# Kernel tuning notes

Measured on AMD Instinct MI355X. Metric: run time of the kernel, lower is better.

The kernel has to match this reference:

```python
import jax, jax.numpy as jnp
import numpy as np

N = 1536       # n_nodes
D_IN = 256     # in_features
D_OUT = 64     # out_features (= n_hidden, n_heads=1, is_concat=True)
N_WAY = 16     # known_attacks_count
SLOPE = 0.2    # LeakyReLU negative slope


def setup_inputs() -> dict:
    key = jax.random.key(0)
    k1, k2, k3, k4, k5 = jax.random.split(key, 5)
    hidden_vectors = jax.random.normal(k1, (N, D_IN), dtype=jnp.float32)
    labels = jax.random.randint(k2, (N, 1), 0, N_WAY)
    zda_mask = jax.random.randint(k3, (N, 1), 0, 2).astype(bool)
    # deterministic support/query split: first half support, last half query
    query_mask = jnp.concatenate([jnp.zeros(N // 2, bool), jnp.ones(N // 2, bool)])
    W = jax.random.normal(k4, (D_OUT, D_IN), jnp.float32) * (1.0 / np.sqrt(D_IN))
    attn_w = jax.random.normal(k5, (D_OUT,), jnp.float32) * (1.0 / np.sqrt(D_OUT))
    return {"hidden_vectors": hidden_vectors, "W": W, "attn_w": attn_w,
            "labels": labels, "zda_mask": zda_mask, "query_mask": query_mask,
            "known_attacks_count": N_WAY}


def _forward(hidden_vectors, W, attn_w, labels, zda_mask, n_way):
    n = hidden_vectors.shape[0]
    dt = hidden_vectors.dtype
    # one-hot labels (scatter equivalent)
    oh = jax.nn.one_hot(labels[:, 0], n_way, dtype=dt)                 # [n, n_way]
    known = ~zda_mask[:, 0]                                            # unknown == zda
    ohm = jnp.where(known[:, None], oh, jnp.zeros((), dt))             # masked one-hot
    # collaborative kernel: semantic similarity between known pairs, else 1
    sem = ohm @ ohm.T                                                  # [n, n]
    cond = known[:, None] & known[None, :]
    kernel = jnp.where(cond, sem, jnp.ones((), dt))
    # GATv2 with shared weights, 1 head: e[i,j] = attn . lrelu(g[i] + g[j])
    g = hidden_vectors @ W.T                                           # [n, d_out]
    s = g[:, None, :] + g[None, :, :]                                  # [n, n, d_out]
    s = jnp.where(s >= 0, s, SLOPE * s)                                # LeakyReLU
    e = jnp.einsum('ijd,d->ij', s, attn_w)                             # [n, n]
    e = jnp.where(kernel == 0.0, -jnp.inf, e)                          # colaborative mask
    a = jax.nn.softmax(e, axis=1)                                      # [n, n]
    h_out = a @ g                                                      # [n, d_out] (concat, 1 head)
    # centroids over support nodes (first half)
    n_sup = n // 2
    h_sup, oh_sup = h_out[:n_sup], oh[:n_sup]
    agg = oh_sup.T @ h_sup                                             # [n_way, d_out]
    counts = oh_sup.sum(0)                                             # [n_way]
    centroids = jnp.where((counts > 0)[:, None],
                          agg / jnp.maximum(counts, 1.0)[:, None], 0.0)
    # inverse euclidean distance scores for query nodes (last half)
    hq = h_out[n_sup:]
    d2 = (jnp.sum(hq * hq, 1)[:, None] + jnp.sum(centroids * centroids, 1)[None, :]
          - 2.0 * hq @ centroids.T)
    dist = jnp.sqrt(jnp.maximum(d2, 0.0))
    scores = 1.0 / (dist + 1e-10)
    return scores, h_out, a


def reference(hidden_vectors, W, attn_w, labels, zda_mask, query_mask, known_attacks_count):
    return _forward(hidden_vectors, W, attn_w, labels, zda_mask, known_attacks_count)
```

## Files before the change

kernel.cpp:

```cpp
#include <hip/hip_runtime.h>
#include <math.h>

#define NN 1536
#define DIN 256
#define DOUT 64
#define NWAY 16
#define NSUP 768
#define IB 12
#define JBLK 256
#define SROWS 6

#define OFF_SCORES 0
#define OFF_H 12288
#define OFF_A 110592

#define WG 0
#define WQ 98304
#define WCODE 99840
#define WCENT 101376

__global__ __launch_bounds__(256) void k_g(const float* __restrict__ hid,
                                           const float* __restrict__ W,
                                           const float* __restrict__ attw,
                                           const int* __restrict__ labels,
                                           const int* __restrict__ zda,
                                           float* __restrict__ g,
                                           float* __restrict__ q,
                                           int* __restrict__ code) {
  int t = threadIdx.x;
  int r = t >> 6, d = t & 63;
  int i = blockIdx.x * 4 + r;
  const float4* hp = (const float4*)(hid + (size_t)i * DIN);
  const float4* wp = (const float4*)(W + (size_t)d * DIN);
  float4 acc = {0.f, 0.f, 0.f, 0.f};
#pragma unroll
  for (int k = 0; k < DIN / 4; k++) {
    float4 h4 = hp[k];
    float4 w4 = wp[k];
    acc.x = fmaf(h4.x, w4.x, acc.x);
    acc.y = fmaf(h4.y, w4.y, acc.y);
    acc.z = fmaf(h4.z, w4.z, acc.z);
    acc.w = fmaf(h4.w, w4.w, acc.w);
  }
  float gv = (acc.x + acc.y) + (acc.z + acc.w);
  g[(size_t)i * DOUT + d] = gv;
  float val = gv * attw[d];
#pragma unroll
  for (int off = 32; off >= 1; off >>= 1) val += __shfl_xor(val, off, 64);
  if (d == 0) q[i] = 0.6f * val;
  if (t < 4) {
    int ii = blockIdx.x * 4 + t;
    code[ii] = zda[ii] ? -1 : labels[ii];
  }
}

__global__ __launch_bounds__(256, 2) void k_e(const float* __restrict__ g,
                                              const float* __restrict__ q,
                                              const int* __restrict__ code,
                                              const float* __restrict__ attw,
                                              float* __restrict__ aout) {
  __shared__ float gis[IB * DOUT];
  __shared__ float lds_p[4][IB][128];
  __shared__ float qi[IB];
  __shared__ int ci[IB];
  int t = threadIdx.x;
  int lane = t & 63;
  int w = t >> 6;
  int whalf = __builtin_amdgcn_readfirstlane(w & 1);
  int jpair = w >> 1;
  int i0 = blockIdx.x * IB;
  int j0 = blockIdx.y * JBLK;
  int jA = j0 + jpair * 128 + lane;
  int jB = jA + 64;

  if (t < IB * 16) {
    ((float4*)gis)[t] = ((const float4*)(g + (size_t)i0 * DOUT))[t];
  } else if (t < IB * 16 + IB) {
    int u = t - IB * 16;
    qi[u] = q[i0 + u];
    ci[u] = code[i0 + u];
  }
  float4 gjA[8], gjB[8];
  {
    const float4* gpA = (const float4*)(g + (size_t)jA * DOUT + whalf * 32);
    const float4* gpB = (const float4*)(g + (size_t)jB * DOUT + whalf * 32);
#pragma unroll
    for (int k = 0; k < 8; k++) gjA[k] = gpA[k];
#pragma unroll
    for (int k = 0; k < 8; k++) gjB[k] = gpB[k];
  }
  const float4* wv = (const float4*)(attw + whalf * 32);
  __syncthreads();

#pragma unroll 1
  for (int u = 0; u < IB; u++) {
    const float4* gv = (const float4*)(gis + u * DOUT + whalf * 32);
    float4 aA = {0.f, 0.f, 0.f, 0.f};
    float4 aB = {0.f, 0.f, 0.f, 0.f};
#pragma unroll
    for (int k = 0; k < 8; k++) {
      float4 a4 = gv[k];
      float4 w4 = wv[k];
      float4 bA = gjA[k];
      float4 bB = gjB[k];
      aA.x = fmaf(w4.x, fabsf(a4.x + bA.x), aA.x);
      aA.y = fmaf(w4.y, fabsf(a4.y + bA.y), aA.y);
      aA.z = fmaf(w4.z, fabsf(a4.z + bA.z), aA.z);
      aA.w = fmaf(w4.w, fabsf(a4.w + bA.w), aA.w);
      aB.x = fmaf(w4.x, fabsf(a4.x + bB.x), aB.x);
      aB.y = fmaf(w4.y, fabsf(a4.y + bB.y), aB.y);
      aB.z = fmaf(w4.z, fabsf(a4.z + bB.z), aB.z);
      aB.w = fmaf(w4.w, fabsf(a4.w + bB.w), aB.w);
    }
    lds_p[w][u][lane] = (aA.x + aA.y) + (aA.z + aA.w);
    lds_p[w][u][lane + 64] = (aB.x + aB.y) + (aB.z + aB.w);
  }
  __syncthreads();

  int jl = t;
  int jp = jl >> 7;
  int sl = jl & 127;
  int jg = j0 + jl;
  float qj = q[jg];
  int cj = code[jg];
#pragma unroll
  for (int u = 0; u < IB; u++) {
    float s = lds_p[2 * jp][u][sl] + lds_p[2 * jp + 1][u][sl];
    float e = (qi[u] + qj) + 0.4f * s;
    int cu = ci[u];
    if ((cu >= 0) && (cj >= 0) && (cu != cj)) e = -1e30f;
    aout[(size_t)(i0 + u) * NN + jg] = e;
  }
}

__global__ __launch_bounds__(512) void k_smh(float* __restrict__ a,
                                             const float* __restrict__ g,
                                             float* __restrict__ h) {
  __shared__ float al[SROWS][NN];
  __shared__ float part[32][SROWS][68];
  __shared__ float red[16];
  int t = threadIdx.x;
  int lane = t & 63;
  int w = t >> 6;
  int r0 = blockIdx.x * SROWS;

#pragma unroll 1
  for (int r = 0; r < SROWS; r++) {
    float* row = a + (size_t)(r0 + r) * NN;
    float v0 = row[t], v1 = row[t + 512], v2 = row[t + 1024];
    float m = fmaxf(fmaxf(v0, v1), v2);
#pragma unroll
    for (int off = 32; off >= 1; off >>= 1) m = fmaxf(m, __shfl_xor(m, off, 64));
    if (lane == 0) red[w] = m;
    __syncthreads();
    m = red[0];
#pragma unroll
    for (int k = 1; k < 8; k++) m = fmaxf(m, red[k]);
    v0 = __expf(v0 - m);
    v1 = __expf(v1 - m);
    v2 = __expf(v2 - m);
    float s = (v0 + v1) + v2;
#pragma unroll
    for (int off = 32; off >= 1; off >>= 1) s += __shfl_xor(s, off, 64);
    if (lane == 0) red[8 + w] = s;
    __syncthreads();
    s = red[8];
#pragma unroll
    for (int k = 1; k < 8; k++) s += red[8 + k];
    float inv = 1.f / s;
    v0 *= inv; v1 *= inv; v2 *= inv;
    al[r][t] = v0; al[r][t + 512] = v1; al[r][t + 1024] = v2;
    row[t] = v0; row[t + 512] = v1; row[t + 1024] = v2;
    __syncthreads();
  }

  int jr = t >> 4;
  int dq = t & 15;
  float4 acc0 = {0,0,0,0}, acc1 = {0,0,0,0}, acc2 = {0,0,0,0};
  float4 acc3 = {0,0,0,0}, acc4 = {0,0,0,0}, acc5 = {0,0,0,0};
#pragma unroll 4
  for (int jj = 0; jj < NN / 32; jj++) {
    int j = jj * 32 + jr;
    float4 g4 = *(const float4*)(g + (size_t)j * DOUT + dq * 4);
    float a0 = al[0][j], a1 = al[1][j], a2 = al[2][j];
    float a3 = al[3][j], a4 = al[4][j], a5 = al[5][j];
    acc0.x = fmaf(a0, g4.x, acc0.x); acc0.y = fmaf(a0, g4.y, acc0.y);
    acc0.z = fmaf(a0, g4.z, acc0.z); acc0.w = fmaf(a0, g4.w, acc0.w);
    acc1.x = fmaf(a1, g4.x, acc1.x); acc1.y = fmaf(a1, g4.y, acc1.y);
    acc1.z = fmaf(a1, g4.z, acc1.z); acc1.w = fmaf(a1, g4.w, acc1.w);
    acc2.x = fmaf(a2, g4.x, acc2.x); acc2.y = fmaf(a2, g4.y, acc2.y);
    acc2.z = fmaf(a2, g4.z, acc2.z); acc2.w = fmaf(a2, g4.w, acc2.w);
    acc3.x = fmaf(a3, g4.x, acc3.x); acc3.y = fmaf(a3, g4.y, acc3.y);
    acc3.z = fmaf(a3, g4.z, acc3.z); acc3.w = fmaf(a3, g4.w, acc3.w);
    acc4.x = fmaf(a4, g4.x, acc4.x); acc4.y = fmaf(a4, g4.y, acc4.y);
    acc4.z = fmaf(a4, g4.z, acc4.z); acc4.w = fmaf(a4, g4.w, acc4.w);
    acc5.x = fmaf(a5, g4.x, acc5.x); acc5.y = fmaf(a5, g4.y, acc5.y);
    acc5.z = fmaf(a5, g4.z, acc5.z); acc5.w = fmaf(a5, g4.w, acc5.w);
  }
  *(float4*)(&part[jr][0][dq * 4]) = acc0;
  *(float4*)(&part[jr][1][dq * 4]) = acc1;
  *(float4*)(&part[jr][2][dq * 4]) = acc2;
  *(float4*)(&part[jr][3][dq * 4]) = acc3;
  *(float4*)(&part[jr][4][dq * 4]) = acc4;
  *(float4*)(&part[jr][5][dq * 4]) = acc5;
  __syncthreads();
  if (t < SROWS * DOUT) {
    int r = t >> 6, d = t & 63;
    float s = 0.f;
#pragma unroll
    for (int k = 0; k < 32; k++) s += part[k][r][d];
    h[(size_t)(r0 + r) * DOUT + d] = s;
  }
}

__global__ __launch_bounds__(1024) void k_cent(const float* __restrict__ h,
                                               const int* __restrict__ labels,
                                               float* __restrict__ cent) {
  __shared__ float part[16][64];
  __shared__ int pc[16];
  int c = blockIdx.x, t = threadIdx.x;
  int d = t & 63, rq = t >> 6;
  float acc = 0.f;
  int cnt = 0;
#pragma unroll 4
  for (int r = rq; r < NSUP; r += 16) {
    int lab = labels[r];
    if (lab == c) { acc += h[(size_t)r * DOUT + d]; cnt++; }
  }
  part[rq][d] = acc;
  if (d == 0) pc[rq] = cnt;
  __syncthreads();
  if (t < 64) {
    float num = 0.f;
    int count = 0;
#pragma unroll
    for (int k = 0; k < 16; k++) { num += part[k][t]; count += pc[k]; }
    cent[c * DOUT + t] = (count > 0) ? (num / (float)count) : 0.f;
  }
}

__global__ __launch_bounds__(256) void k_scores(const float* __restrict__ h,
                                                const float* __restrict__ cent,
                                                float* __restrict__ scores) {
  __shared__ float cl[NWAY * 65];
  __shared__ float hl[16 * 65];
  int t = threadIdx.x;
  int q0 = blockIdx.x * 16;
#pragma unroll
  for (int u = 0; u < 4; u++) {
    int f = t + u * 256;
    int row = f >> 6, k = f & 63;
    cl[row * 65 + k] = cent[f];
    hl[row * 65 + k] = h[(size_t)(NSUP + q0) * DOUT + f];
  }
  __syncthreads();
  int qr = t >> 4, c = t & 15;
  const float* hv = hl + qr * 65;
  const float* cv = cl + c * 65;
  float hh = 0.f, cc = 0.f, hc = 0.f;
#pragma unroll
  for (int k = 0; k < DOUT; k++) {
    float av = hv[k], bv = cv[k];
    hh = fmaf(av, av, hh);
    cc = fmaf(bv, bv, cc);
    hc = fmaf(av, bv, hc);
  }
  float d2 = fmaxf(hh + cc - 2.f * hc, 0.f);
  scores[q0 * NWAY + t] = 1.f / (sqrtf(d2) + 1e-10f);
}

extern "C" void kernel_launch(void* const* d_in, const int* in_sizes, int n_in,
                              void* d_out, int out_size, void* d_ws, size_t ws_size,
                              hipStream_t stream) {
  const float* hid = (const float*)d_in[0];
  const float* W = (const float*)d_in[1];
  const float* attw = (const float*)d_in[2];
  const int* labels = (const int*)d_in[3];
  const int* zda = (const int*)d_in[4];
  float* out = (float*)d_out;
  float* ws = (float*)d_ws;

  float* g = ws + WG;
  float* q = ws + WQ;
  int* code = (int*)(ws + WCODE);
  float* cent = ws + WCENT;
  float* scores = out + OFF_SCORES;
  float* h = out + OFF_H;
  float* a = out + OFF_A;

  hipLaunchKernelGGL(k_g, dim3(NN / 4), dim3(256), 0, stream, hid, W, attw, labels, zda, g, q, code);
  hipLaunchKernelGGL(k_e, dim3(NN / IB, NN / JBLK), dim3(256), 0, stream, g, q, code, attw, a);
  hipLaunchKernelGGL(k_smh, dim3(NN / SROWS), dim3(512), 0, stream, a, g, h);
  hipLaunchKernelGGL(k_cent, dim3(NWAY), dim3(1024), 0, stream, h, labels, cent);
  hipLaunchKernelGGL(k_scores, dim3(NSUP / 16), dim3(256), 0, stream, h, cent, scores);
}
```

Baseline: 73.28 us.

## Split k_e feature dim across four waves and halve softmax rows per block

In the attention-score kernel, each wave now handles a 16-feature quarter for all 256 columns instead of a 32-feature half for 128 columns. This changes the register tiling and LDS partial-sum layout, and the four partials are summed per column. The softmax/aggregation kernel processes 3 rows per block instead of 6, doubling the grid and reusing one LDS buffer for both the probability rows and the partial sums to cut shared memory and raise occupancy. The trade-off is more blocks re-reading g and an extra barrier.

Result: faster. 70.10 us (-4.3%).

```diff
diff --git a/kernel.cpp b/kernel.cpp
--- a/kernel.cpp
+++ b/kernel.cpp
@@ -8,7 +8,7 @@
 #define NSUP 768
 #define IB 12
 #define JBLK 256
-#define SROWS 6
+#define SROWS 3
 
 #define OFF_SCORES 0
 #define OFF_H 12288
@@ -60,18 +60,15 @@
                                               const float* __restrict__ attw,
                                               float* __restrict__ aout) {
   __shared__ float gis[IB * DOUT];
-  __shared__ float lds_p[4][IB][128];
+  __shared__ float lp[4][IB][JBLK];
   __shared__ float qi[IB];
   __shared__ int ci[IB];
   int t = threadIdx.x;
   int lane = t & 63;
   int w = t >> 6;
-  int whalf = __builtin_amdgcn_readfirstlane(w & 1);
-  int jpair = w >> 1;
+  int wq = __builtin_amdgcn_readfirstlane(w);
   int i0 = blockIdx.x * IB;
   int j0 = blockIdx.y * JBLK;
-  int jA = j0 + jpair * 128 + lane;
-  int jB = jA + 64;
 
   if (t < IB * 16) {
     ((float4*)gis)[t] = ((const float4*)(g + (size_t)i0 * DOUT))[t];
@@ -80,52 +77,67 @@
     qi[u] = q[i0 + u];
     ci[u] = code[i0 + u];
   }
-  float4 gjA[8], gjB[8];
+  float4 gj0[4], gj1[4], gj2[4], gj3[4];
   {
-    const float4* gpA = (const float4*)(g + (size_t)jA * DOUT + whalf * 32);
-    const float4* gpB = (const float4*)(g + (size_t)jB * DOUT + whalf * 32);
-#pragma unroll
-    for (int k = 0; k < 8; k++) gjA[k] = gpA[k];
-#pragma unroll
-    for (int k = 0; k < 8; k++) gjB[k] = gpB[k];
-  }
-  const float4* wv = (const float4*)(attw + whalf * 32);
+    const float4* p0 = (const float4*)(g + (size_t)(j0 + lane) * DOUT + wq * 16);
+    const float4* p1 = (const float4*)(g + (size_t)(j0 + 64 + lane) * DOUT + wq * 16);
+    const float4* p2 = (const float4*)(g + (size_t)(j0 + 128 + lane) * DOUT + wq * 16);
+    const float4* p3 = (const float4*)(g + (size_t)(j0 + 192 + lane) * DOUT + wq * 16);
+#pragma unroll
+    for (int k = 0; k < 4; k++) gj0[k] = p0[k];
+#pragma unroll
+    for (int k = 0; k < 4; k++) gj1[k] = p1[k];
+#pragma unroll
+    for (int k = 0; k < 4; k++) gj2[k] = p2[k];
+#pragma unroll
+    for (int k = 0; k < 4; k++) gj3[k] = p3[k];
+  }
+  const float4* wv = (const float4*)(attw + wq * 16);
   __syncthreads();
 
 #pragma unroll 1
   for (int u = 0; u < IB; u++) {
-    const float4* gv = (const float4*)(gis + u * DOUT + whalf * 32);
-    float4 aA = {0.f, 0.f, 0.f, 0.f};
-    float4 aB = {0.f, 0.f, 0.f, 0.f};
-#pragma unroll
-    for (int k = 0; k < 8; k++) {
+    const float4* gv = (const float4*)(gis + u * DOUT + wq * 16);
+    float4 a0 = {0,0,0,0}, a1 = {0,0,0,0}, a2 = {0,0,0,0}, a3 = {0,0,0,0};
+#pragma unroll
+    for (int k = 0; k < 4; k++) {
       float4 a4 = gv[k];
       float4 w4 = wv[k];
-      float4 bA = gjA[k];
-      float4 bB = gjB[k];
-      aA.x = fmaf(w4.x, fabsf(a4.x + bA.x), aA.x);
-      aA.y = fmaf(w4.y, fabsf(a4.y + bA.y), aA.y);
-      aA.z = fmaf(w4.z, fabsf(a4.z + bA.z), aA.z);
-      aA.w = fmaf(w4.w, fabsf(a4.w + bA.w), aA.w);
-      aB.x = fmaf(w4.x, fabsf(a4.x + bB.x), aB.x);
-      aB.y = fmaf(w4.y, fabsf(a4.y + bB.y), aB.y);
-      aB.z = fmaf(w4.z, fabsf(a4.z + bB.z), aB.z);
-      aB.w = fmaf(w4.w, fabsf(a4.w + bB.w), aB.w);
+      float4 b;
+      b = gj0[k];
+      a0.x = fmaf(w4.x, fabsf(a4.x + b.x), a0.x);
+      a0.y = fmaf(w4.y, fabsf(a4.y + b.y), a0.y);
+      a0.z = fmaf(w4.z, fabsf(a4.z + b.z), a0.z);
+      a0.w = fmaf(w4.w, fabsf(a4.w + b.w), a0.w);
+      b = gj1[k];
+      a1.x = fmaf(w4.x, fabsf(a4.x + b.x), a1.x);
+      a1.y = fmaf(w4.y, fabsf(a4.y + b.y), a1.y);
+      a1.z = fmaf(w4.z, fabsf(a4.z + b.z), a1.z);
+      a1.w = fmaf(w4.w, fabsf(a4.w + b.w), a1.w);
+      b = gj2[k];
+      a2.x = fmaf(w4.x, fabsf(a4.x + b.x), a2.x);
+      a2.y = fmaf(w4.y, fabsf(a4.y + b.y), a2.y);
+      a2.z = fmaf(w4.z, fabsf(a4.z + b.z), a2.z);
+      a2.w = fmaf(w4.w, fabsf(a4.w + b.w), a2.w);
+      b = gj3[k];
+      a3.x = fmaf(w4.x, fabsf(a4.x + b.x), a3.x);
+      a3.y = fmaf(w4.y, fabsf(a4.y + b.y), a3.y);
+      a3.z = fmaf(w4.z, fabsf(a4.z + b.z), a3.z);
+      a3.w = fmaf(w4.w, fabsf(a4.w + b.w), a3.w);
     }
-    lds_p[w][u][lane] = (aA.x + aA.y) + (aA.z + aA.w);
-    lds_p[w][u][lane + 64] = (aB.x + aB.y) + (aB.z + aB.w);
-  }
-  __syncthreads();
-
-  int jl = t;
-  int jp = jl >> 7;
-  int sl = jl & 127;
-  int jg = j0 + jl;
+    lp[w][u][lane] = (a0.x + a0.y) + (a0.z + a0.w);
+    lp[w][u][lane + 64] = (a1.x + a1.y) + (a1.z + a1.w);
+    lp[w][u][lane + 128] = (a2.x + a2.y) + (a2.z + a2.w);
+    lp[w][u][lane + 192] = (a3.x + a3.y) + (a3.z + a3.w);
+  }
+  __syncthreads();
+
+  int jg = j0 + t;
   float qj = q[jg];
   int cj = code[jg];
 #pragma unroll
   for (int u = 0; u < IB; u++) {
-    float s = lds_p[2 * jp][u][sl] + lds_p[2 * jp + 1][u][sl];
+    float s = (lp[0][u][t] + lp[1][u][t]) + (lp[2][u][t] + lp[3][u][t]);
     float e = (qi[u] + qj) + 0.4f * s;
     int cu = ci[u];
     if ((cu >= 0) && (cj >= 0) && (cu != cj)) e = -1e30f;
@@ -136,9 +148,9 @@
 __global__ __launch_bounds__(512) void k_smh(float* __restrict__ a,
                                              const float* __restrict__ g,
                                              float* __restrict__ h) {
-  __shared__ float al[SROWS][NN];
-  __shared__ float part[32][SROWS][68];
+  __shared__ float buf[32 * SROWS * 68];
   __shared__ float red[16];
+  float* al = buf;
   int t = threadIdx.x;
   int lane = t & 63;
   int w = t >> 6;
@@ -169,7 +181,7 @@
     for (int k = 1; k < 8; k++) s += red[8 + k];
     float inv = 1.f / s;
     v0 *= inv; v1 *= inv; v2 *= inv;
-    al[r][t] = v0; al[r][t + 512] = v1; al[r][t + 1024] = v2;
+    al[r * NN + t] = v0; al[r * NN + 512 + t] = v1; al[r * NN + 1024 + t] = v2;
     row[t] = v0; row[t + 512] = v1; row[t + 1024] = v2;
     __syncthreads();
   }
@@ -177,38 +189,28 @@
   int jr = t >> 4;
   int dq = t & 15;
   float4 acc0 = {0,0,0,0}, acc1 = {0,0,0,0}, acc2 = {0,0,0,0};
-  float4 acc3 = {0,0,0,0}, acc4 = {0,0,0,0}, acc5 = {0,0,0,0};
 #pragma unroll 4
   for (int jj = 0; jj < NN / 32; jj++) {
     int j = jj * 32 + jr;
     float4 g4 = *(const float4*)(g + (size_t)j * DOUT + dq * 4);
-    float a0 = al[0][j], a1 = al[1][j], a2 = al[2][j];
-    float a3 = al[3][j], a4 = al[4][j], a5 = al[5][j];
+    float a0 = al[j], a1 = al[NN + j], a2 = al[2 * NN + j];
     acc0.x = fmaf(a0, g4.x, acc0.x); acc0.y = fmaf(a0, g4.y, acc0.y);
     acc0.z = fmaf(a0, g4.z, acc0.z); acc0.w = fmaf(a0, g4.w, acc0.w);
     acc1.x = fmaf(a1, g4.x, acc1.x); acc1.y = fmaf(a1, g4.y, acc1.y);
     acc1.z = fmaf(a1, g4.z, acc1.z); acc1.w = fmaf(a1, g4.w, acc1.w);
     acc2.x = fmaf(a2, g4.x, acc2.x); acc2.y = fmaf(a2, g4.y, acc2.y);
     acc2.z = fmaf(a2, g4.z, acc2.z); acc2.w = fmaf(a2, g4.w, acc2.w);
-    acc3.x = fmaf(a3, g4.x, acc3.x); acc3.y = fmaf(a3, g4.y, acc3.y);
-    acc3.z = fmaf(a3, g4.z, acc3.z); acc3.w = fmaf(a3, g4.w, acc3.w);
-    acc4.x = fmaf(a4, g4.x, acc4.x); acc4.y = fmaf(a4, g4.y, acc4.y);
-    acc4.z = fmaf(a4, g4.z, acc4.z); acc4.w = fmaf(a4, g4.w, acc4.w);
-    acc5.x = fmaf(a5, g4.x, acc5.x); acc5.y = fmaf(a5, g4.y, acc5.y);
-    acc5.z = fmaf(a5, g4.z, acc5.z); acc5.w = fmaf(a5, g4.w, acc5.w);
-  }
-  *(float4*)(&part[jr][0][dq * 4]) = acc0;
-  *(float4*)(&part[jr][1][dq * 4]) = acc1;
-  *(float4*)(&part[jr][2][dq * 4]) = acc2;
-  *(float4*)(&part[jr][3][dq * 4]) = acc3;
-  *(float4*)(&part[jr][4][dq * 4]) = acc4;
-  *(float4*)(&part[jr][5][dq * 4]) = acc5;
+  }
+  __syncthreads();
+  *(float4*)(&buf[(jr * SROWS + 0) * 68 + dq * 4]) = acc0;
+  *(float4*)(&buf[(jr * SROWS + 1) * 68 + dq * 4]) = acc1;
+  *(float4*)(&buf[(jr * SROWS + 2) * 68 + dq * 4]) = acc2;
   __syncthreads();
   if (t < SROWS * DOUT) {
     int r = t >> 6, d = t & 63;
     float s = 0.f;
 #pragma unroll
-    for (int k = 0; k < 32; k++) s += part[k][r][d];
+    for (int k = 0; k < 32; k++) s += buf[(k * SROWS + r) * 68 + d];
     h[(size_t)(r0 + r) * DOUT + d] = s;
   }
 }
```
